# Optimization experiments

Measured on AMD Instinct MI355X. Metric: run time of the kernel, lower is better.

## Reference

```python
import jax, jax.numpy as jnp
import numpy as np

N = 20000
IN_CH, HID, OUT_CH = 512, 64, 16
H1, H2 = 8, 1
NEG_SLOPE = 0.2


def setup_inputs() -> dict:
    key = jax.random.key(0)
    ks = jax.random.split(key, 10)
    E = 320000
    x = jax.random.normal(ks[0], (N, IN_CH), dtype=jnp.float32)
    edge_index = jax.random.randint(ks[1], (2, E), 0, N, dtype=jnp.int64)
    s = 0.05
    return {
        "x": x,
        "edge_index": edge_index,
        "W1": jax.random.normal(ks[2], (H1 * HID, IN_CH), dtype=jnp.float32) * s,
        "att_src1": jax.random.normal(ks[3], (1, H1, HID), dtype=jnp.float32) * s,
        "att_dst1": jax.random.normal(ks[4], (1, H1, HID), dtype=jnp.float32) * s,
        "b1": jnp.zeros((H1 * HID,), dtype=jnp.float32),
        "W2": jax.random.normal(ks[5], (H2 * OUT_CH, H1 * HID), dtype=jnp.float32) * s,
        "att_src2": jax.random.normal(ks[6], (1, H2, OUT_CH), dtype=jnp.float32) * s,
        "att_dst2": jax.random.normal(ks[7], (1, H2, OUT_CH), dtype=jnp.float32) * s,
        "b2": jnp.zeros((OUT_CH,), dtype=jnp.float32),
    }


def _gat_conv(x, src, dst, W, att_src, att_dst, bias, heads, out_ch, concat):
    # Linear transform: [N, H, C]
    h = (x @ W.T).reshape(x.shape[0], heads, out_ch)
    n = x.shape[0]
    # Per-node attention logits (a_src . h), (a_dst . h): [N, H]
    a_s = (h * att_src).sum(-1)
    a_d = (h * att_dst).sum(-1)
    # Edge-wise LeakyReLU attention: [E, H]
    e = a_s[src] + a_d[dst]
    e = jnp.where(e >= 0, e, NEG_SLOPE * e)
    # Segment softmax over incoming edges of each destination node
    m = jax.ops.segment_max(e, dst, num_segments=n)
    p = jnp.exp(e - m[dst])
    z = jax.ops.segment_sum(p, dst, num_segments=n)
    alpha = p / z[dst]  # [E, H]
    # Weighted scatter-aggregate: out[dst] += alpha * h[src]
    msg = h[src] * alpha[:, :, None]  # [E, H, C]
    out = jax.ops.segment_sum(msg, dst, num_segments=n)
    out = out.reshape(n, heads * out_ch) if concat else out.mean(axis=1)
    return out + bias


def reference(x, edge_index, W1, att_src1, att_dst1, b1, W2, att_src2, att_dst2, b2):
    # PyG GATConv adds self-loops by default
    loops = jnp.arange(N, dtype=edge_index.dtype)
    src = jnp.concatenate([edge_index[0], loops])
    dst = jnp.concatenate([edge_index[1], loops])
    # dropout layers are identity in eval mode
    h = _gat_conv(x, src, dst, W1, att_src1, att_dst1, b1, H1, HID, True)
    h = jax.nn.relu(h)
    out = _gat_conv(h, src, dst, W2, att_src2, att_dst2, b2, H2, OUT_CH, False)
    return out
```

## Files before the change

### kernel.cpp

```cpp
#include <hip/hip_runtime.h>

#define Nn     20000
#define IN_CH  512
#define C1     512
#define H1n    8
#define HIDn   64
#define OUT_CH 16
#define En     320000
#define EPn    340000
#define NEG    0.2f

typedef __attribute__((ext_vector_type(8))) short bf16x8;
typedef __attribute__((ext_vector_type(4))) float f32x4;

__device__ inline unsigned short bf16_rne(float f) {
  unsigned int u = __float_as_uint(f);
  return (unsigned short)((u + 0x7fffu + ((u >> 16) & 1u)) >> 16);
}
__device__ inline float bf16_f(unsigned short u) {
  return __uint_as_float(((unsigned int)u) << 16);
}

__device__ inline bf16x8 pack8(float4 f0, float4 f1) {
  unsigned int r0, r1, r2, r3;
  asm("v_cvt_pk_bf16_f32 %0, %1, %2" : "=v"(r0) : "v"(f0.x), "v"(f0.y));
  asm("v_cvt_pk_bf16_f32 %0, %1, %2" : "=v"(r1) : "v"(f0.z), "v"(f0.w));
  asm("v_cvt_pk_bf16_f32 %0, %1, %2" : "=v"(r2) : "v"(f1.x), "v"(f1.y));
  asm("v_cvt_pk_bf16_f32 %0, %1, %2" : "=v"(r3) : "v"(f1.z), "v"(f1.w));
  union { unsigned int u[4]; bf16x8 v; } un;
  un.u[0] = r0; un.u[1] = r1; un.u[2] = r2; un.u[3] = r3;
  return un.v;
}

#define NW8  (C1 * IN_CH / 8)
#define NW28 (OUT_CH * C1 / 8)
#define NH4  (EPn / 4)
__global__ __launch_bounds__(256) void cvtwh_kernel(
    const float* __restrict__ W1, unsigned short* __restrict__ w1b,
    const float* __restrict__ W2, unsigned short* __restrict__ w2b,
    const int* __restrict__ ei, int* __restrict__ cnt)
{
  int i = blockIdx.x * 256 + threadIdx.x;
  const float* in; unsigned short* ob; int idx;
  if (i < NW8) { in = W1; ob = w1b; idx = i; }
  else if (i < NW8 + NW28) { in = W2; ob = w2b; idx = i - NW8; }
  else if (i < NW8 + NW28 + NH4) {
    int e4 = (i - NW8 - NW28) * 4;
    if (e4 < En) {
      int4 dv = *(const int4*)&ei[En + e4];
      atomicAdd(&cnt[dv.x], 1); atomicAdd(&cnt[dv.y], 1);
      atomicAdd(&cnt[dv.z], 1); atomicAdd(&cnt[dv.w], 1);
    } else {
      int d = e4 - En;
      atomicAdd(&cnt[d], 1);     atomicAdd(&cnt[d + 1], 1);
      atomicAdd(&cnt[d + 2], 1); atomicAdd(&cnt[d + 3], 1);
    }
    return;
  } else return;
  float4 f0 = ((const float4*)in)[idx * 2];
  float4 f1 = ((const float4*)in)[idx * 2 + 1];
  float f[8] = {f0.x, f0.y, f0.z, f0.w, f1.x, f1.y, f1.z, f1.w};
  unsigned short h[8];
#pragma unroll
  for (int j = 0; j < 8; j++) h[j] = bf16_rne(f[j]);
  ushort4 hv0 = {h[0], h[1], h[2], h[3]}, hv1 = {h[4], h[5], h[6], h[7]};
  ((ushort4*)ob)[idx * 2] = hv0; ((ushort4*)ob)[idx * 2 + 1] = hv1;
}

#define GLL(gp, lp) __builtin_amdgcn_global_load_lds( \
    (const __attribute__((address_space(1))) void*)(gp), \
    (__attribute__((address_space(3))) void*)(lp), 16, 0, 0)

#define SWZ(c)  ((c) ^ (((c) >> 3) & 3))
#define SWZA(c) ((c) ^ (((c) >> 3) & 7))

__global__ __launch_bounds__(256, 3) void gemm1_mfma(
    const float* __restrict__ Af, const unsigned short* __restrict__ Bb,
    const float* __restrict__ attS, const float* __restrict__ attD,
    unsigned short* __restrict__ Cb, float* __restrict__ as1, float* __restrict__ ad1)
{
  __shared__ float sAf[2][128 * 32];
  __shared__ unsigned short sB[2][128 * 32];
  int t = threadIdx.x;
  int wgid = blockIdx.x;
  int bm = (wgid & 7) + 8 * (wgid >> 5);
  int bn = (wgid >> 3) & 3;
  if (bm >= 157) return;
  int lane = t & 63, w = t >> 6;

  int acb[4]; size_t aoff[4];
#pragma unroll
  for (int q = 0; q < 4; q++) {
    int slot = w * 256 + q * 64 + lane;
    acb[q] = w * 256 + q * 64;
    int cs = SWZA(slot);
    int ra = bm * 128 + (cs >> 3); if (ra > Nn - 1) ra = Nn - 1;
    aoff[q] = (size_t)ra * IN_CH + (cs & 7) * 4;
  }
  int slot0 = w * 128 + lane, slot1 = slot0 + 64;
  int bcb0 = w * 128, bcb1 = w * 128 + 64;
  int cs0 = SWZ(slot0), cs1 = SWZ(slot1);
  int br0 = bn * 128 + (cs0 >> 2);
  int br1 = bn * 128 + (cs1 >> 2);
  size_t offB0 = (size_t)br0 * IN_CH + (cs0 & 3) * 8;
  size_t offB1 = (size_t)br1 * IN_CH + (cs1 & 3) * 8;

  int wm = (w >> 1) * 64, wn = (w & 1) * 64;
  int lr = lane & 15, kb = lane >> 4;

  f32x4 acc[4][4] = {};

  GLL(Af + aoff[0], sAf[0] + acb[0] * 4);
  GLL(Af + aoff[1], sAf[0] + acb[1] * 4);
  GLL(Af + aoff[2], sAf[0] + acb[2] * 4);
  GLL(Af + aoff[3], sAf[0] + acb[3] * 4);
  GLL(Bb + offB0, sB[0] + bcb0 * 8);
  GLL(Bb + offB1, sB[0] + bcb1 * 8);
  __syncthreads();

#pragma unroll 2
  for (int it = 0; it < 16; it++) {
    int cur = it & 1;
    const float* Ac = sAf[cur];
    const unsigned short* Bc = sB[cur];
    bf16x8 ah[4], bh[4];
#pragma unroll
    for (int i = 0; i < 4; i++) {
      int c0 = (wm + i * 16 + lr) * 8 + kb * 2;
      float4 f0 = *(const float4*)&Ac[SWZA(c0) * 4];
      float4 f1 = *(const float4*)&Ac[SWZA(c0 + 1) * 4];
      ah[i] = pack8(f0, f1);
      int rcb = (wn + i * 16 + lr) * 4 + kb;
      bh[i] = *(const bf16x8*)&Bc[SWZ(rcb) * 8];
    }
    if (it < 15) {
      int k1 = (it + 1) * 32;
      float* An = sAf[cur ^ 1];
      unsigned short* Bn = sB[cur ^ 1];
      GLL(Af + aoff[0] + k1, An + acb[0] * 4);
      GLL(Af + aoff[1] + k1, An + acb[1] * 4);
      GLL(Af + aoff[2] + k1, An + acb[2] * 4);
      GLL(Af + aoff[3] + k1, An + acb[3] * 4);
      GLL(Bb + offB0 + k1, Bn + bcb0 * 8);
      GLL(Bb + offB1 + k1, Bn + bcb1 * 8);
    }
#pragma unroll
    for (int i = 0; i < 4; i++)
#pragma unroll
      for (int j = 0; j < 4; j++)
        acc[i][j] = __builtin_amdgcn_mfma_f32_16x16x32_bf16(ah[i], bh[j], acc[i][j], 0, 0, 0);
    __syncthreads();
  }

  int lq = lane >> 4;
#pragma unroll
  for (int i = 0; i < 4; i++) {
    int r0 = bm * 128 + wm + i * 16 + lq * 4;
#pragma unroll
    for (int j = 0; j < 4; j++) {
      int ccol = bn * 128 + wn + j * 16 + lr;
#pragma unroll
      for (int q = 0; q < 4; q++) {
        unsigned int myv = bf16_rne(acc[i][j][q]);
        unsigned int pv = __shfl_xor(myv, 1);
        int r = r0 + q;
        if (!(lr & 1) && r < Nn) {
          unsigned int word = myv | (pv << 16);
          *(unsigned int*)&Cb[(size_t)r * C1 + ccol] = word;
        }
      }
    }
  }
  int hh = bn * 2 + (wn >> 6);
  float aSj[4], aDj[4];
#pragma unroll
  for (int j = 0; j < 4; j++) {
    int cc = bn * 128 + wn + j * 16 + lr;
    aSj[j] = attS[cc]; aDj[j] = attD[cc];
  }
#pragma unroll
  for (int i = 0; i < 4; i++)
#pragma unroll
    for (int q = 0; q < 4; q++) {
      float s = acc[i][0][q] * aSj[0] + acc[i][1][q] * aSj[1]
              + acc[i][2][q] * aSj[2] + acc[i][3][q] * aSj[3];
      float dd = acc[i][0][q] * aDj[0] + acc[i][1][q] * aDj[1]
               + acc[i][2][q] * aDj[2] + acc[i][3][q] * aDj[3];
#pragma unroll
      for (int off = 1; off < 16; off <<= 1) {
        s += __shfl_xor(s, off);
        dd += __shfl_xor(dd, off);
      }
      int r = bm * 128 + wm + i * 16 + lq * 4 + q;
      if (lr == 0 && r < Nn) { as1[r * 8 + hh] = s; ad1[r * 8 + hh] = dd; }
    }
}

__global__ __launch_bounds__(1024) void scan_kernel(
    const int* __restrict__ cnt, int* __restrict__ row)
{
  extern __shared__ int sm[];
  __shared__ int wsum[16];
  int t = threadIdx.x;

  for (int i = t; i < Nn; i += 1024) {
    int c = i / 20, o = i - c * 20;
    sm[c * 21 + o] = cnt[i];
  }
  __syncthreads();

  int v[20];
  int s = 0;
  if (t < 1000) {
    int base = t * 21;
#pragma unroll
    for (int j = 0; j < 20; j++) {
      int c = sm[base + j];
      v[j] = s;
      s += c;
    }
  }
  int lane = t & 63, w = t >> 6;
  int incl = s;
#pragma unroll
  for (int off = 1; off < 64; off <<= 1) {
    int o = __shfl_up(incl, off);
    if (lane >= off) incl += o;
  }
  if (lane == 63) wsum[w] = incl;
  __syncthreads();
  if (w == 0) {
    int ws = (lane < 16) ? wsum[lane] : 0;
#pragma unroll
    for (int off = 1; off < 16; off <<= 1) {
      int o = __shfl_up(ws, off);
      if (lane >= off) ws += o;
    }
    if (lane < 16) wsum[lane] = ws;
  }
  __syncthreads();
  int excl = ((w > 0) ? wsum[w - 1] : 0) + incl - s;
  if (t < 1000) {
    int base = t * 21;
#pragma unroll
    for (int j = 0; j < 20; j++) sm[base + j] = excl + v[j];
  }
  __syncthreads();
  for (int i = t; i < Nn; i += 1024) {
    int c = i / 20, o = i - c * 20;
    row[i] = sm[c * 21 + o];
  }
  if (t == 0) row[Nn] = EPn;
}

__global__ void scatter_kernel(const int* __restrict__ ei, const int* __restrict__ row,
                               int* __restrict__ cur, int* __restrict__ csr)
{
  int e4 = (blockIdx.x * 256 + threadIdx.x) * 4;
  if (e4 >= EPn) return;
  if (e4 < En) {
    int4 sv = *(const int4*)&ei[e4];
    int4 dv = *(const int4*)&ei[En + e4];
    int sa[4] = {sv.x, sv.y, sv.z, sv.w};
    int da[4] = {dv.x, dv.y, dv.z, dv.w};
#pragma unroll
    for (int j = 0; j < 4; j++) {
      int pos = row[da[j]] + atomicAdd(&cur[da[j]], 1);
      csr[pos] = sa[j];
    }
  } else {
#pragma unroll
    for (int j = 0; j < 4; j++) {
      int d = e4 - En + j;
      int pos = row[d] + atomicAdd(&cur[d], 1);
      csr[pos] = d;
    }
  }
}

__global__ __launch_bounds__(256, 6) void agg1_kernel(
    const int* __restrict__ row, const int* __restrict__ csr,
    const unsigned short* __restrict__ h1b, const float* __restrict__ as1,
    const float* __restrict__ adv, const float* __restrict__ b1,
    const unsigned short* __restrict__ W2b,
    const float* __restrict__ attS2, const float* __restrict__ attD2,
    float* __restrict__ h2, float* __restrict__ as2, float* __restrict__ ad2)
{
  __shared__ float part[2][64 * 9];

  int t = threadIdx.x, lane = t & 63, w = t >> 6;
  int pr = w >> 1;
  int p  = w & 1;
  int d = blockIdx.x * 2 + pr;
  int beg = row[d], end = row[d + 1];
  int deg = end - beg;
  int hq = lane >> 3;
  size_t chb = (size_t)8 * lane;
  float adH = adv[d * 8 + hq];

  float a0 = 0.f, a1 = 0.f, a2 = 0.f, a3 = 0.f;
  float a4 = 0.f, a5 = 0.f, a6 = 0.f, a7 = 0.f;
  float z = 0.f;
  int nj = (deg - p + 1) >> 1;
#pragma unroll 4
  for (int j = 0; j < nj; j++) {
    int e = beg + p + 2 * j;
    int s = csr[e];
    float v = as1[s * 8 + hq] + adH;
    v = (v >= 0.f) ? v : NEG * v;
    float pp = __expf(v);
    z += pp;
    uint4 u = *(const uint4*)&h1b[(size_t)s * C1 + chb];
    a0 = fmaf(pp, __uint_as_float(u.x << 16), a0);
    a1 = fmaf(pp, __uint_as_float(u.x & 0xffff0000u), a1);
    a2 = fmaf(pp, __uint_as_float(u.y << 16), a2);
    a3 = fmaf(pp, __uint_as_float(u.y & 0xffff0000u), a3);
    a4 = fmaf(pp, __uint_as_float(u.z << 16), a4);
    a5 = fmaf(pp, __uint_as_float(u.z & 0xffff0000u), a5);
    a6 = fmaf(pp, __uint_as_float(u.w << 16), a6);
    a7 = fmaf(pp, __uint_as_float(u.w & 0xffff0000u), a7);
  }

  if (p == 1) {
    float* ps = &part[pr][lane * 9];
    ps[0] = a0; ps[1] = a1; ps[2] = a2; ps[3] = a3;
    ps[4] = a4; ps[5] = a5; ps[6] = a6; ps[7] = a7; ps[8] = z;
  }
  __syncthreads();
  if (p == 0) {
    const float* ps = &part[pr][lane * 9];
    a0 += ps[0]; a1 += ps[1]; a2 += ps[2]; a3 += ps[3];
    a4 += ps[4]; a5 += ps[5]; a6 += ps[6]; a7 += ps[7]; z += ps[8];
    float rz = 1.f / z;
    float4 b0 = *(const float4*)&b1[chb];
    float4 b4 = *(const float4*)&b1[chb + 4];
    float o0 = fmaf(a0, rz, b0.x); o0 = o0 > 0.f ? o0 : 0.f;
    float o1 = fmaf(a1, rz, b0.y); o1 = o1 > 0.f ? o1 : 0.f;
    float o2 = fmaf(a2, rz, b0.z); o2 = o2 > 0.f ? o2 : 0.f;
    float o3 = fmaf(a3, rz, b0.w); o3 = o3 > 0.f ? o3 : 0.f;
    float o4 = fmaf(a4, rz, b4.x); o4 = o4 > 0.f ? o4 : 0.f;
    float o5 = fmaf(a5, rz, b4.y); o5 = o5 > 0.f ? o5 : 0.f;
    float o6 = fmaf(a6, rz, b4.z); o6 = o6 > 0.f ? o6 : 0.f;
    float o7 = fmaf(a7, rz, b4.w); o7 = o7 > 0.f ? o7 : 0.f;

    float myh2 = 0.f, s2 = 0.f, d2 = 0.f;
#pragma unroll
    for (int j = 0; j < OUT_CH; j++) {
      bf16x8 wv = *(const bf16x8*)&W2b[j * 512 + chb];
      float pj = o0 * bf16_f((unsigned short)wv[0]) + o1 * bf16_f((unsigned short)wv[1])
               + o2 * bf16_f((unsigned short)wv[2]) + o3 * bf16_f((unsigned short)wv[3])
               + o4 * bf16_f((unsigned short)wv[4]) + o5 * bf16_f((unsigned short)wv[5])
               + o6 * bf16_f((unsigned short)wv[6]) + o7 * bf16_f((unsigned short)wv[7]);
#pragma unroll
      for (int off = 1; off < 64; off <<= 1) pj += __shfl_xor(pj, off);
      if (lane == j) myh2 = pj;
      s2 = fmaf(pj, attS2[j], s2);
      d2 = fmaf(pj, attD2[j], d2);
    }
    if (lane < OUT_CH) h2[(size_t)d * OUT_CH + lane] = myh2;
    if (lane == 0) { as2[d] = s2; ad2[d] = d2; }
  }
}

__global__ __launch_bounds__(256) void agg2_kernel(
    const int* __restrict__ row, const int* __restrict__ csr,
    const float* __restrict__ h2, const float* __restrict__ as2,
    const float* __restrict__ ad2, const float* __restrict__ b2,
    float* __restrict__ out)
{
  int wave = threadIdx.x >> 6, lane = threadIdx.x & 63;
  int d = blockIdx.x * 4 + wave;
  int beg = row[d], end = row[d + 1];
  float add = ad2[d];

  int c = lane & 15;
  float acc = 0.f, z = 0.f;
  for (int e = beg + (lane >> 4); e < end; e += 4) {
    int s = csr[e];
    float v = as2[s] + add;
    v = (v >= 0.f) ? v : NEG * v;
    float p = __expf(v);
    z += p;
    acc = fmaf(p, h2[(size_t)s * 16 + c], acc);
  }
  acc += __shfl_xor(acc, 16);
  acc += __shfl_xor(acc, 32);
  z += __shfl_xor(z, 16);
  z += __shfl_xor(z, 32);
  if (lane < 16) out[(size_t)d * 16 + lane] = acc / z + b2[lane];
}

extern "C" void kernel_launch(void* const* d_in, const int* in_sizes, int n_in,
                              void* d_out, int out_size, void* d_ws, size_t ws_size,
                              hipStream_t stream)
{
  const float* x    = (const float*)d_in[0];
  const int*   ei   = (const int*)d_in[1];
  const float* W1   = (const float*)d_in[2];
  const float* asv1 = (const float*)d_in[3];
  const float* adv1 = (const float*)d_in[4];
  const float* b1   = (const float*)d_in[5];
  const float* W2   = (const float*)d_in[6];
  const float* asv2 = (const float*)d_in[7];
  const float* adv2 = (const float*)d_in[8];
  const float* b2   = (const float*)d_in[9];
  float* out = (float*)d_out;

  unsigned short* h1b = (unsigned short*)d_ws;
  unsigned short* w_b = h1b + (size_t)Nn * C1;
  unsigned short* w2b = w_b + (size_t)C1 * IN_CH;
  float* as1   = (float*)(w2b + (size_t)OUT_CH * C1);
  float* ad1   = as1 + (size_t)Nn * H1n;
  float* h2    = ad1 + (size_t)Nn * H1n;
  float* as2   = h2 + (size_t)Nn * OUT_CH;
  float* ad2   = as2 + Nn;
  int* csr  = (int*)(ad2 + Nn);
  int* cnt  = csr + EPn;
  int* cur  = cnt + Nn;
  int* rowp = cur + Nn;

  hipMemsetAsync(cnt, 0, 2 * Nn * sizeof(int), stream);

  cvtwh_kernel<<<(NW8 + NW28 + NH4 + 255) / 256, 256, 0, stream>>>(
      W1, w_b, W2, w2b, ei, cnt);

  gemm1_mfma<<<640, 256, 0, stream>>>(x, w_b, asv1, adv1, h1b, as1, ad1);

  scan_kernel<<<1, 1024, 1000 * 21 * sizeof(int), stream>>>(cnt, rowp);
  scatter_kernel<<<(EPn / 4 + 255) / 256, 256, 0, stream>>>(ei, rowp, cur, csr);
  agg1_kernel<<<Nn / 2, 256, 0, stream>>>(rowp, csr, h1b, as1, ad1, b1,
                                          w2b, asv2, adv2, h2, as2, ad2);
  agg2_kernel<<<Nn / 4, 256, 0, stream>>>(rowp, csr, h2, as2, ad2, b2, out);
}
```

Before: 140.8 us.

## Split layer-1 aggregation per head across blocks with atomic second-layer projection

The layer-1 aggregation kernel now uses one wave per (destination node, head) instead of two waves sharing all heads of a node. Each lane handles two channels of one head, and the two edge halves are reduced with a shuffle instead of shared memory and a barrier. Each head's partial contribution to the layer-2 projection and attention logits is combined with atomicAdd into zero-initialised buffers, so the memset now clears h2/as2/ad2 together with the counters. The aim is more parallelism and less per-thread register pressure, at the cost of 8x more blocks, narrower 4-byte gathers, 8x repeated CSR/logit reads and global atomics.

Result: slower. 270.0 us (+91.8%).

```diff
diff --git a/kernel.cpp b/kernel.cpp
--- a/kernel.cpp
+++ b/kernel.cpp
@@ -278,7 +278,7 @@
   }
 }
 
-__global__ __launch_bounds__(256, 6) void agg1_kernel(
+__global__ __launch_bounds__(256) void agg1_kernel(
     const int* __restrict__ row, const int* __restrict__ csr,
     const unsigned short* __restrict__ h1b, const float* __restrict__ as1,
     const float* __restrict__ adv, const float* __restrict__ b1,
@@ -286,79 +286,55 @@
     const float* __restrict__ attS2, const float* __restrict__ attD2,
     float* __restrict__ h2, float* __restrict__ as2, float* __restrict__ ad2)
 {
-  __shared__ float part[2][64 * 9];
-
+  int wgid = blockIdx.x;
+  int h  = wgid & 7;
+  int dg = wgid >> 3;
   int t = threadIdx.x, lane = t & 63, w = t >> 6;
-  int pr = w >> 1;
-  int p  = w & 1;
-  int d = blockIdx.x * 2 + pr;
+  int d = dg * 4 + w;
   int beg = row[d], end = row[d + 1];
-  int deg = end - beg;
-  int hq = lane >> 3;
-  size_t chb = (size_t)8 * lane;
-  float adH = adv[d * 8 + hq];
-
-  float a0 = 0.f, a1 = 0.f, a2 = 0.f, a3 = 0.f;
-  float a4 = 0.f, a5 = 0.f, a6 = 0.f, a7 = 0.f;
-  float z = 0.f;
-  int nj = (deg - p + 1) >> 1;
-#pragma unroll 4
-  for (int j = 0; j < nj; j++) {
-    int e = beg + p + 2 * j;
+  int eo = lane >> 5;
+  int c2 = lane & 31;
+  int ch = h * 64 + 2 * c2;
+  float adH = adv[d * 8 + h];
+
+  float a0 = 0.f, a1 = 0.f, z = 0.f;
+  for (int e = beg + eo; e < end; e += 2) {
     int s = csr[e];
-    float v = as1[s * 8 + hq] + adH;
+    float v = as1[s * 8 + h] + adH;
     v = (v >= 0.f) ? v : NEG * v;
-    float pp = __expf(v);
-    z += pp;
-    uint4 u = *(const uint4*)&h1b[(size_t)s * C1 + chb];
-    a0 = fmaf(pp, __uint_as_float(u.x << 16), a0);
-    a1 = fmaf(pp, __uint_as_float(u.x & 0xffff0000u), a1);
-    a2 = fmaf(pp, __uint_as_float(u.y << 16), a2);
-    a3 = fmaf(pp, __uint_as_float(u.y & 0xffff0000u), a3);
-    a4 = fmaf(pp, __uint_as_float(u.z << 16), a4);
-    a5 = fmaf(pp, __uint_as_float(u.z & 0xffff0000u), a5);
-    a6 = fmaf(pp, __uint_as_float(u.w << 16), a6);
-    a7 = fmaf(pp, __uint_as_float(u.w & 0xffff0000u), a7);
-  }
-
-  if (p == 1) {
-    float* ps = &part[pr][lane * 9];
-    ps[0] = a0; ps[1] = a1; ps[2] = a2; ps[3] = a3;
-    ps[4] = a4; ps[5] = a5; ps[6] = a6; ps[7] = a7; ps[8] = z;
-  }
-  __syncthreads();
-  if (p == 0) {
-    const float* ps = &part[pr][lane * 9];
-    a0 += ps[0]; a1 += ps[1]; a2 += ps[2]; a3 += ps[3];
-    a4 += ps[4]; a5 += ps[5]; a6 += ps[6]; a7 += ps[7]; z += ps[8];
-    float rz = 1.f / z;
-    float4 b0 = *(const float4*)&b1[chb];
-    float4 b4 = *(const float4*)&b1[chb + 4];
-    float o0 = fmaf(a0, rz, b0.x); o0 = o0 > 0.f ? o0 : 0.f;
-    float o1 = fmaf(a1, rz, b0.y); o1 = o1 > 0.f ? o1 : 0.f;
-    float o2 = fmaf(a2, rz, b0.z); o2 = o2 > 0.f ? o2 : 0.f;
-    float o3 = fmaf(a3, rz, b0.w); o3 = o3 > 0.f ? o3 : 0.f;
-    float o4 = fmaf(a4, rz, b4.x); o4 = o4 > 0.f ? o4 : 0.f;
-    float o5 = fmaf(a5, rz, b4.y); o5 = o5 > 0.f ? o5 : 0.f;
-    float o6 = fmaf(a6, rz, b4.z); o6 = o6 > 0.f ? o6 : 0.f;
-    float o7 = fmaf(a7, rz, b4.w); o7 = o7 > 0.f ? o7 : 0.f;
-
-    float myh2 = 0.f, s2 = 0.f, d2 = 0.f;
-#pragma unroll
-    for (int j = 0; j < OUT_CH; j++) {
-      bf16x8 wv = *(const bf16x8*)&W2b[j * 512 + chb];
-      float pj = o0 * bf16_f((unsigned short)wv[0]) + o1 * bf16_f((unsigned short)wv[1])
-               + o2 * bf16_f((unsigned short)wv[2]) + o3 * bf16_f((unsigned short)wv[3])
-               + o4 * bf16_f((unsigned short)wv[4]) + o5 * bf16_f((unsigned short)wv[5])
-               + o6 * bf16_f((unsigned short)wv[6]) + o7 * bf16_f((unsigned short)wv[7]);
-#pragma unroll
-      for (int off = 1; off < 64; off <<= 1) pj += __shfl_xor(pj, off);
-      if (lane == j) myh2 = pj;
-      s2 = fmaf(pj, attS2[j], s2);
-      d2 = fmaf(pj, attD2[j], d2);
-    }
-    if (lane < OUT_CH) h2[(size_t)d * OUT_CH + lane] = myh2;
-    if (lane == 0) { as2[d] = s2; ad2[d] = d2; }
+    float p = __expf(v);
+    z += p;
+    unsigned int u = *(const unsigned int*)&h1b[(size_t)s * C1 + ch];
+    a0 = fmaf(p, __uint_as_float(u << 16), a0);
+    a1 = fmaf(p, __uint_as_float(u & 0xffff0000u), a1);
+  }
+  a0 += __shfl_xor(a0, 32);
+  a1 += __shfl_xor(a1, 32);
+  z  += __shfl_xor(z, 32);
+
+  float rz = 1.f / z;
+  float o0 = fmaf(a0, rz, b1[ch]);     o0 = o0 > 0.f ? o0 : 0.f;
+  float o1 = fmaf(a1, rz, b1[ch + 1]); o1 = o1 > 0.f ? o1 : 0.f;
+
+  float s2 = 0.f, d2 = 0.f, myj = 0.f;
+#pragma unroll
+  for (int j = 0; j < OUT_CH; j++) {
+    unsigned int wu = *(const unsigned int*)&W2b[j * 512 + ch];
+    float pj = o0 * __uint_as_float(wu << 16)
+             + o1 * __uint_as_float(wu & 0xffff0000u);
+    pj += __shfl_xor(pj, 1);
+    pj += __shfl_xor(pj, 2);
+    pj += __shfl_xor(pj, 4);
+    pj += __shfl_xor(pj, 8);
+    pj += __shfl_xor(pj, 16);
+    if (c2 == j) myj = pj;
+    s2 = fmaf(pj, attS2[j], s2);
+    d2 = fmaf(pj, attD2[j], d2);
+  }
+  if (eo == 0) {
+    if (c2 < OUT_CH) atomicAdd(&h2[(size_t)d * OUT_CH + c2], myj);
+    else if (c2 == 16) atomicAdd(&as2[d], s2);
+    else if (c2 == 17) atomicAdd(&ad2[d], d2);
   }
 }
 
@@ -414,12 +390,12 @@
   float* h2    = ad1 + (size_t)Nn * H1n;
   float* as2   = h2 + (size_t)Nn * OUT_CH;
   float* ad2   = as2 + Nn;
-  int* csr  = (int*)(ad2 + Nn);
-  int* cnt  = csr + EPn;
+  int* cnt  = (int*)(ad2 + Nn);
   int* cur  = cnt + Nn;
   int* rowp = cur + Nn;
-
-  hipMemsetAsync(cnt, 0, 2 * Nn * sizeof(int), stream);
+  int* csr  = rowp + Nn + 1;
+
+  hipMemsetAsync(h2, 0, (size_t)Nn * 20 * sizeof(float), stream);
 
   cvtwh_kernel<<<(NW8 + NW28 + NH4 + 255) / 256, 256, 0, stream>>>(
       W1, w_b, W2, w2b, ei, cnt);
@@ -428,7 +404,7 @@
 
   scan_kernel<<<1, 1024, 1000 * 21 * sizeof(int), stream>>>(cnt, rowp);
   scatter_kernel<<<(EPn / 4 + 255) / 256, 256, 0, stream>>>(ei, rowp, cur, csr);
-  agg1_kernel<<<Nn / 2, 256, 0, stream>>>(rowp, csr, h1b, as1, ad1, b1,
-                                          w2b, asv2, adv2, h2, as2, ad2);
+  agg1_kernel<<<(Nn / 4) * 8, 256, 0, stream>>>(rowp, csr, h1b, as1, ad1, b1,
+                                                w2b, asv2, adv2, h2, as2, ad2);
   agg2_kernel<<<Nn / 4, 256, 0, stream>>>(rowp, csr, h2, as2, ad2, b2, out);
 }
```
